# Optimization experiments

Hardware: AMD Instinct MI355X
Metric: run time of the kernel (lower is better)

The kernel has to match this reference:

```python
import jax, jax.numpy as jnp
import numpy as np

D_MODEL, D_STATE, D_CONV, D_INNER, DT_RANK = 1024, 16, 4, 2048, 64
B_SZ, L = 4, 2048

def setup_inputs() -> dict:
    key = jax.random.key(0)
    ks = jax.random.split(key, 7)
    return {
        "hidden_states": jax.random.normal(ks[0], (B_SZ, L, D_MODEL), jnp.float32),
        "in_proj_w": jax.random.normal(ks[1], (2 * D_INNER, D_MODEL), jnp.float32) * (D_MODEL ** -0.5),
        "conv_w": jax.random.normal(ks[2], (D_INNER, 1, D_CONV), jnp.float32) * 0.5,
        "conv_b": jax.random.normal(ks[3], (D_INNER,), jnp.float32) * 0.1,
        "x_proj_w": jax.random.normal(ks[4], (DT_RANK + 2 * D_STATE, D_INNER), jnp.float32) * (D_INNER ** -0.5),
        "dt_proj_w": jax.random.normal(ks[5], (D_INNER, DT_RANK), jnp.float32) * (DT_RANK ** -0.5),
        "A_log": jax.random.uniform(ks[6], (D_INNER, D_STATE), jnp.float32, 0.0, 2.0),
    }

def reference(hidden_states, in_proj_w, conv_w, conv_b, x_proj_w, dt_proj_w, A_log):
    b, l, d = hidden_states.shape
    # in_proj: (b,l,d) x (2*d_inner,d)^T -> (b, 2*d_inner, l)
    xz = jnp.einsum('bld,ed->bel', hidden_states, in_proj_w)
    x, z = jnp.split(xz, 2, axis=1)  # each (b, d_inner, l); z unused downstream
    A = -jnp.exp(A_log)              # (d_inner, d_state)
    # causal depthwise conv1d (left pad d_conv-1) + SiLU
    x = jax.lax.conv_general_dilated(
        x, conv_w, window_strides=(1,), padding=[(D_CONV - 1, 0)],
        feature_group_count=D_INNER,
        dimension_numbers=('NCH', 'OIH', 'NCH'))
    x = jax.nn.silu(x + conv_b[None, :, None])  # (b, d_inner, l)
    # x_proj: (b,l,dt_rank+2*d_state)
    x_dbl = jnp.einsum('bdl,ed->ble', x, x_proj_w)
    dt, B_mat, C_mat = jnp.split(x_dbl, [DT_RANK, DT_RANK + D_STATE], axis=-1)
    dt = jnp.einsum('blr,dr->bdl', dt, dt_proj_w)          # (b, d_inner, l), no bias
    B_mat = jnp.swapaxes(B_mat, 1, 2)                      # (b, d_state, l)
    C_mat = jnp.swapaxes(C_mat, 1, 2)                      # (b, d_state, l)
    return (dt, A, B_mat, C_mat, x)
```

## Files before the change

### kernel.cpp

```cpp
#include <hip/hip_runtime.h>
#include <hip/hip_bf16.h>
#include <math.h>

#define D_MODEL 1024
#define D_STATE 16
#define D_CONV  4
#define D_INNER 2048
#define DT_RANK 64
#define B_SZ    4
#define L_SEQ   2048

#define OFF_DT 0
#define OFF_A  (B_SZ * D_INNER * L_SEQ)
#define OFF_B  (OFF_A + D_INNER * D_STATE)
#define OFF_C  (OFF_B + B_SZ * D_STATE * L_SEQ)
#define OFF_X  (OFF_C + B_SZ * D_STATE * L_SEQ)

typedef __attribute__((ext_vector_type(8))) short bf16x8;
typedef __attribute__((ext_vector_type(8))) unsigned short us8;
typedef __attribute__((ext_vector_type(4))) float f32x4;
typedef unsigned short ushort_t;
typedef unsigned int uint_t;

static __device__ __forceinline__ ushort_t f2bf(float f) {
  __hip_bfloat16 h = __float2bfloat16(f);
  return *(ushort_t*)&h;
}
static __device__ __forceinline__ float bf2f(ushort_t u) {
  union { uint_t u; float f; } c;
  c.u = ((uint_t)u) << 16;
  return c.f;
}

#define N4_HS   (B_SZ * L_SEQ * D_MODEL / 4)
#define N4_W    (D_INNER * D_MODEL / 4)
#define N4_XW   ((DT_RANK + 2 * D_STATE) * D_INNER / 4)
#define N4_DW   (D_INNER * DT_RANK / 4)
#define N4_Z0   (B_SZ * DT_RANK * L_SEQ / 4)
#define N4_Z1   (2 * B_SZ * D_STATE * L_SEQ / 4)
#define N4_A    (D_INNER * D_STATE / 4)
#define N4_TOT  (N4_HS + N4_W + N4_XW + N4_DW + N4_Z0 + N4_Z1 + N4_A)

__global__ __launch_bounds__(256) void k_prep(
    const float4* __restrict__ hs, const float4* __restrict__ ipw,
    const float4* __restrict__ xpw, const float4* __restrict__ dpw,
    const float4* __restrict__ alog,
    ushort4* __restrict__ bfHS, ushort4* __restrict__ bfW,
    ushort4* __restrict__ xwb, ushort4* __restrict__ dwb,
    float4* __restrict__ z0, float4* __restrict__ z1,
    float4* __restrict__ aout) {
  int i = blockIdx.x * 256 + threadIdx.x;
  if (i < N4_HS) {
    float4 v = hs[i];
    ushort4 o; o.x = f2bf(v.x); o.y = f2bf(v.y); o.z = f2bf(v.z); o.w = f2bf(v.w);
    bfHS[i] = o;
    return;
  }
  i -= N4_HS;
  if (i < N4_W) {
    float4 v = ipw[i];
    ushort4 o; o.x = f2bf(v.x); o.y = f2bf(v.y); o.z = f2bf(v.z); o.w = f2bf(v.w);
    bfW[i] = o;
    return;
  }
  i -= N4_W;
  if (i < N4_XW) {
    float4 v = xpw[i];
    ushort4 o; o.x = f2bf(v.x); o.y = f2bf(v.y); o.z = f2bf(v.z); o.w = f2bf(v.w);
    xwb[i] = o;
    return;
  }
  i -= N4_XW;
  if (i < N4_DW) {
    float4 v = dpw[i];
    ushort4 o; o.x = f2bf(v.x); o.y = f2bf(v.y); o.z = f2bf(v.z); o.w = f2bf(v.w);
    dwb[i] = o;
    return;
  }
  i -= N4_DW;
  if (i < N4_Z0) { z0[i] = (float4){0.f, 0.f, 0.f, 0.f}; return; }
  i -= N4_Z0;
  if (i < N4_Z1) { z1[i] = (float4){0.f, 0.f, 0.f, 0.f}; return; }
  i -= N4_Z1;
  if (i < N4_A) {
    float4 v = alog[i];
    float4 o;
    o.x = -expf(v.x); o.y = -expf(v.y); o.z = -expf(v.z); o.w = -expf(v.w);
    aout[i] = o;
  }
}

__global__ __launch_bounds__(512, 2) void k_inproj_mfma(
    const ushort_t* __restrict__ Wb,
    const ushort_t* __restrict__ HSb,
    ushort_t* __restrict__ Cout) {
  const int flat = blockIdx.x + 8 * blockIdx.y + 64 * blockIdx.z;
  const int swz  = (flat & 7) * 32 + (flat >> 3);
  const int bn = swz & 7;
  const int bm = (swz >> 3) & 7;
  const int b  = swz >> 6;

  __shared__ ushort_t sh[65536];
  const int tid  = threadIdx.x;
  const int w    = tid >> 6;
  const int lane = tid & 63;
  const int wm = w >> 2, wn = w & 3;
  const int ksel = lane >> 4;
  const int frow = lane & 15;
  const int sr = tid >> 2;
  const int ss = tid & 3;

  const ushort_t* Ag = Wb + (size_t)(bm * 256) * D_MODEL;
  const ushort_t* Bg = HSb + (size_t)b * L_SEQ * D_MODEL
                           + (size_t)(bn * 256) * D_MODEL;

  f32x4 acc[8][4];
#pragma unroll
  for (int m = 0; m < 8; ++m)
#pragma unroll
    for (int n = 0; n < 4; ++n) acc[m][n] = (f32x4){0.f, 0.f, 0.f, 0.f};

  const int sxs = ss ^ ((sr >> 1) & 3);

#define STAGE(BUF, T)                                                            \
  do {                                                                           \
    _Pragma("unroll")                                                            \
    for (int mh = 0; mh < 4; ++mh) {                                             \
      const ushort_t* gbase = (mh < 2) ? Ag : Bg;                                \
      const ushort_t* grow = gbase + (size_t)((mh & 1) * 128 + sr) * D_MODEL     \
                                   + (T) * 64 + sxs * 8;                         \
      _Pragma("unroll")                                                          \
      for (int q = 0; q < 2; ++q) {                                              \
        ushort_t* dst = sh + (BUF) * 32768 + (mh >> 1) * 16384                   \
                           + (mh & 1) * 8192 + q * 4096 + tid * 8;               \
        __builtin_amdgcn_global_load_lds(                                        \
            (const __attribute__((address_space(1))) void*)(grow + q * 32),      \
            (__attribute__((address_space(3))) void*)dst, 16, 0, 0);             \
      }                                                                          \
    }                                                                            \
  } while (0)

#define COMPUTE(BUF)                                                             \
  do {                                                                           \
    _Pragma("unroll")                                                            \
    for (int ks = 0; ks < 2; ++ks) {                                             \
      bf16x8 af[8], bfr[4];                                                      \
      _Pragma("unroll")                                                          \
      for (int m = 0; m < 8; ++m) {                                              \
        int r = m * 16 + frow;                                                   \
        af[m] = *(const bf16x8*)(sh + (BUF) * 32768 + wm * 8192 + ks * 4096      \
                                 + (r * 4 + (ksel ^ ((r >> 1) & 3))) * 8);       \
      }                                                                          \
      _Pragma("unroll")                                                          \
      for (int n = 0; n < 4; ++n) {                                              \
        int ll = wn * 64 + n * 16 + frow;                                        \
        int h = ll >> 7, r = ll & 127;                                           \
        bfr[n] = *(const bf16x8*)(sh + (BUF) * 32768 + 16384 + h * 8192          \
                                  + ks * 4096                                    \
                                  + (r * 4 + (ksel ^ ((r >> 1) & 3))) * 8);      \
      }                                                                          \
      __builtin_amdgcn_s_setprio(1);                                             \
      _Pragma("unroll")                                                          \
      for (int m = 0; m < 8; ++m)                                                \
        _Pragma("unroll")                                                        \
        for (int n = 0; n < 4; ++n)                                              \
          acc[m][n] = __builtin_amdgcn_mfma_f32_16x16x32_bf16(af[m], bfr[n],     \
                                                              acc[m][n], 0, 0, 0); \
      __builtin_amdgcn_s_setprio(0);                                             \
    }                                                                            \
  } while (0)

  STAGE(0, 0);
  STAGE(1, 1);
  asm volatile("s_waitcnt vmcnt(8)" ::: "memory");
  __builtin_amdgcn_s_barrier();

  for (int t = 0; t < 14; ++t) {
    COMPUTE(t & 1);
    __builtin_amdgcn_sched_barrier(0);
    __builtin_amdgcn_s_barrier();
    STAGE(t & 1, t + 2);
    asm volatile("s_waitcnt vmcnt(8)" ::: "memory");
    __builtin_amdgcn_s_barrier();
    __builtin_amdgcn_sched_barrier(0);
  }
  COMPUTE(0);
  __builtin_amdgcn_sched_barrier(0);
  __builtin_amdgcn_s_barrier();
  asm volatile("s_waitcnt vmcnt(0)" ::: "memory");
  __builtin_amdgcn_s_barrier();
  COMPUTE(1);
#undef STAGE
#undef COMPUTE

  __syncthreads();

  const int crow0 = (lane >> 4) * 4;
  const int ccol  = lane & 15;
  ushort_t* Cb = Cout + (size_t)b * D_INNER * L_SEQ;
#pragma unroll
  for (int p = 0; p < 2; ++p) {
    if (wm == p) {
#pragma unroll
      for (int m = 0; m < 8; ++m)
#pragma unroll
        for (int n = 0; n < 4; ++n) {
          int r0 = m * 16 + crow0;
          int c  = wn * 64 + n * 16 + ccol;
#pragma unroll
          for (int i = 0; i < 4; ++i)
            sh[(r0 + i) * 272 + c] = f2bf(acc[m][n][i]);
        }
    }
    __syncthreads();
#pragma unroll
    for (int q = 0; q < 8; ++q) {
      int idx = q * 512 + tid;
      int r   = idx >> 5;
      int c8  = idx & 31;
      us8 v = *(const us8*)(sh + r * 272 + c8 * 8);
      *(us8*)(Cb + (size_t)(bm * 256 + p * 128 + r) * L_SEQ + bn * 256 + c8 * 8) = v;
    }
    __syncthreads();
  }
}

__global__ __launch_bounds__(256) void k_xproj_fused(
    const ushort_t* __restrict__ XWb,
    const ushort_t* __restrict__ Xpre,
    const float* __restrict__ CW,
    const float* __restrict__ CB,
    float* __restrict__ Xout,
    float* __restrict__ XDBL,
    float* __restrict__ OutB,
    float* __restrict__ OutC) {
  const int ln = blockIdx.x;
  const int sk = blockIdx.y;
  const int b  = blockIdx.z;
  __shared__ ushort_t As[96 * 40];
  __shared__ ushort_t Bs[64 * 34];
  const int tid  = threadIdx.x;
  const int wv   = tid >> 6;
  const int lane = tid & 63;
  const int wr = wv >> 1, wc = wv & 1;
  const int ksel = lane >> 4;
  const int frow = lane & 15;

  f32x4 acc[3][2];
#pragma unroll
  for (int i = 0; i < 3; ++i)
#pragma unroll
    for (int j = 0; j < 2; ++j) acc[i][j] = (f32x4){0.f, 0.f, 0.f, 0.f};

  for (int k0 = 0; k0 < 512; k0 += 32) {
    const int koff = sk * 512 + k0;
    {
      int row = tid >> 2, s = tid & 3;
      bf16x8 v = *(const bf16x8*)(XWb + (size_t)row * D_INNER + koff + s * 8);
      *(bf16x8*)(As + row * 40 + s * 8) = v;
      if (tid < 128) {
        int row2 = 64 + (tid >> 2);
        bf16x8 v2 = *(const bf16x8*)(XWb + (size_t)row2 * D_INNER + koff + s * 8);
        *(bf16x8*)(As + row2 * 40 + s * 8) = v2;
      }
    }
    {
      int n4 = tid & 15;
      int kp = tid >> 4;
      int l0 = ln * 64 + 4 * n4;
      float sv[2][4];
#pragma unroll
      for (int r = 0; r < 2; ++r) {
        int d = koff + 2 * kp + r;
        const ushort_t* row = Xpre + ((size_t)b * D_INNER + d) * L_SEQ;
        ushort4 cur = *(const ushort4*)(row + l0);
        float em3 = 0.f, em2 = 0.f, em1 = 0.f;
        if (l0 >= 4) {
          ushort4 pv = *(const ushort4*)(row + l0 - 4);
          em3 = bf2f(pv.y); em2 = bf2f(pv.z); em1 = bf2f(pv.w);
        }
        float ee[7] = {em3, em2, em1, bf2f(cur.x), bf2f(cur.y), bf2f(cur.z), bf2f(cur.w)};
        float4 w = *(const float4*)(CW + d * 4);
        float bias = CB[d];
#pragma unroll
        for (int i = 0; i < 4; ++i) {
          float v = w.x * ee[i] + w.y * ee[i + 1] + w.z * ee[i + 2] + w.w * ee[i + 3] + bias;
          sv[r][i] = v / (1.f + expf(-v));
        }
        *(float4*)(Xout + ((size_t)b * D_INNER + d) * L_SEQ + l0) =
            make_float4(sv[r][0], sv[r][1], sv[r][2], sv[r][3]);
      }
#pragma unroll
      for (int i = 0; i < 4; ++i) {
        uint_t pk = (uint_t)f2bf(sv[0][i]) | ((uint_t)f2bf(sv[1][i]) << 16);
        *(uint_t*)(Bs + (4 * n4 + i) * 34 + 2 * kp) = pk;
      }
    }
    __syncthreads();

    bf16x8 af[3], bfr[2];
#pragma unroll
    for (int mi = 0; mi < 3; ++mi) {
      int row = wr * 48 + mi * 16 + frow;
      af[mi] = *(const bf16x8*)(As + row * 40 + ksel * 8);
    }
#pragma unroll
    for (int ni = 0; ni < 2; ++ni) {
      int n = wc * 32 + ni * 16 + frow;
      const uint_t* p = (const uint_t*)(Bs + n * 34);
      union { uint_t u[4]; bf16x8 v; } fr;
#pragma unroll
      for (int q = 0; q < 4; ++q) fr.u[q] = p[ksel * 4 + q];
      bfr[ni] = fr.v;
    }
#pragma unroll
    for (int mi = 0; mi < 3; ++mi)
#pragma unroll
      for (int ni = 0; ni < 2; ++ni)
        acc[mi][ni] = __builtin_amdgcn_mfma_f32_16x16x32_bf16(af[mi], bfr[ni], acc[mi][ni], 0, 0, 0);
    __syncthreads();
  }

  const int crow0 = (lane >> 4) * 4;
  const int ccol  = lane & 15;
#pragma unroll
  for (int mi = 0; mi < 3; ++mi) {
    int e0 = wr * 48 + mi * 16 + crow0;
    float* base;
    int eoff;
    if (e0 < 64)      { base = XDBL + (size_t)b * 64 * L_SEQ; eoff = e0; }
    else if (e0 < 80) { base = OutB + (size_t)b * D_STATE * L_SEQ; eoff = e0 - 64; }
    else              { base = OutC + (size_t)b * D_STATE * L_SEQ; eoff = e0 - 80; }
#pragma unroll
    for (int ni = 0; ni < 2; ++ni) {
      int l = ln * 64 + wc * 32 + ni * 16 + ccol;
#pragma unroll
      for (int r = 0; r < 4; ++r)
        atomicAdd(base + (size_t)(eoff + r) * L_SEQ + l, acc[mi][ni][r]);
    }
  }
}

__global__ __launch_bounds__(256) void k_dt_mfma(
    const ushort_t* __restrict__ DWb,
    const float* __restrict__ XDBL,
    float* __restrict__ DT) {
  const int ln = blockIdx.x;
  const int dm = blockIdx.y;
  const int b  = blockIdx.z;
  __shared__ ushort_t As[128 * 72];
  __shared__ ushort_t Bs[128 * 68];
  const int tid  = threadIdx.x;
  const int wv   = tid >> 6;
  const int lane = tid & 63;
  const int wr = wv >> 1, wc = wv & 1;
  const int ksel = lane >> 4;
  const int frow = lane & 15;

#pragma unroll
  for (int q = 0; q < 4; ++q) {
    int u = tid + 256 * q;
    int row = u >> 3, s = u & 7;
    *(bf16x8*)(As + row * 72 + s * 8) =
        *(const bf16x8*)(DWb + (size_t)(dm * 128 + row) * DT_RANK + s * 8);
  }
#pragma unroll
  for (int q = 0; q < 4; ++q) {
    int u = tid + 256 * q;
    int n4 = u & 31;
    int kp = u >> 5;
    const float* g = XDBL + ((size_t)b * DT_RANK + 2 * kp) * L_SEQ + ln * 128 + 4 * n4;
    float4 x0 = *(const float4*)g;
    float4 x1 = *(const float4*)(g + L_SEQ);
    float e0[4] = {x0.x, x0.y, x0.z, x0.w};
    float e1[4] = {x1.x, x1.y, x1.z, x1.w};
#pragma unroll
    for (int i = 0; i < 4; ++i) {
      uint_t pk = (uint_t)f2bf(e0[i]) | ((uint_t)f2bf(e1[i]) << 16);
      *(uint_t*)(Bs + (4 * n4 + i) * 68 + 2 * kp) = pk;
    }
  }
  __syncthreads();

  f32x4 acc[4][4];
#pragma unroll
  for (int i = 0; i < 4; ++i)
#pragma unroll
    for (int j = 0; j < 4; ++j) acc[i][j] = (f32x4){0.f, 0.f, 0.f, 0.f};

#pragma unroll
  for (int ks = 0; ks < 2; ++ks) {
    bf16x8 af[4], bfr[4];
#pragma unroll
    for (int m = 0; m < 4; ++m) {
      int row = wr * 64 + m * 16 + frow;
      af[m] = *(const bf16x8*)(As + row * 72 + ks * 32 + ksel * 8);
    }
#pragma unroll
    for (int n = 0; n < 4; ++n) {
      int nn = wc * 64 + n * 16 + frow;
      bfr[n] = *(const bf16x8*)(Bs + nn * 68 + ks * 32 + ksel * 8);
    }
#pragma unroll
    for (int m = 0; m < 4; ++m)
#pragma unroll
      for (int n = 0; n < 4; ++n)
        acc[m][n] = __builtin_amdgcn_mfma_f32_16x16x32_bf16(af[m], bfr[n], acc[m][n], 0, 0, 0);
  }

  const int crow0 = (lane >> 4) * 4;
  const int ccol  = lane & 15;
  float* Cb = DT + (size_t)b * D_INNER * L_SEQ;
#pragma unroll
  for (int m = 0; m < 4; ++m) {
    int gr0 = dm * 128 + wr * 64 + m * 16 + crow0;
#pragma unroll
    for (int n = 0; n < 4; ++n) {
      int gc = ln * 128 + wc * 64 + n * 16 + ccol;
#pragma unroll
      for (int i = 0; i < 4; ++i)
        Cb[(size_t)(gr0 + i) * L_SEQ + gc] = acc[m][n][i];
    }
  }
}

extern "C" void kernel_launch(void* const* d_in, const int* in_sizes, int n_in,
                              void* d_out, int out_size, void* d_ws, size_t ws_size,
                              hipStream_t stream) {
  const float* hs   = (const float*)d_in[0];
  const float* ipw  = (const float*)d_in[1];
  const float* cw   = (const float*)d_in[2];
  const float* cb   = (const float*)d_in[3];
  const float* xpw  = (const float*)d_in[4];
  const float* dpw  = (const float*)d_in[5];
  const float* alog = (const float*)d_in[6];

  float* out    = (float*)d_out;
  float* dt_out = out + OFF_DT;
  float* a_out  = out + OFF_A;
  float* b_out  = out + OFF_B;
  float* c_out  = out + OFF_C;
  float* x_out  = out + OFF_X;

  unsigned short* bfHS = (unsigned short*)x_out;
  unsigned short* bfW  = bfHS + (size_t)B_SZ * L_SEQ * D_MODEL;
  unsigned short* xpre = (unsigned short*)dt_out;
  float* xdbl = (float*)d_ws;
  unsigned short* xwb = (unsigned short*)((char*)d_ws + 2097152);
  unsigned short* dwb = (unsigned short*)((char*)d_ws + 2097152 + 393216);

  k_prep<<<dim3((N4_TOT + 255) / 256), 256, 0, stream>>>(
      (const float4*)hs, (const float4*)ipw, (const float4*)xpw,
      (const float4*)dpw, (const float4*)alog,
      (ushort4*)bfHS, (ushort4*)bfW, (ushort4*)xwb, (ushort4*)dwb,
      (float4*)xdbl, (float4*)b_out, (float4*)a_out);

  k_inproj_mfma<<<dim3(8, 8, 4), 512, 0, stream>>>(bfW, bfHS, xpre);
  k_xproj_fused<<<dim3(32, 4, 4), 256, 0, stream>>>(xwb, xpre, cw, cb,
                                                    x_out, xdbl, b_out, c_out);
  k_dt_mfma<<<dim3(16, 16, 4), 256, 0, stream>>>(dwb, xdbl, dt_out);
}
```

Measured before the change: 119.8 us.

## Replace split-K atomics in x_proj with partial buffers reduced in dt kernel

```diff
diff --git a/kernel.cpp b/kernel.cpp
--- a/kernel.cpp
+++ b/kernel.cpp
@@ -36,10 +36,8 @@
 #define N4_W    (D_INNER * D_MODEL / 4)
 #define N4_XW   ((DT_RANK + 2 * D_STATE) * D_INNER / 4)
 #define N4_DW   (D_INNER * DT_RANK / 4)
-#define N4_Z0   (B_SZ * DT_RANK * L_SEQ / 4)
-#define N4_Z1   (2 * B_SZ * D_STATE * L_SEQ / 4)
 #define N4_A    (D_INNER * D_STATE / 4)
-#define N4_TOT  (N4_HS + N4_W + N4_XW + N4_DW + N4_Z0 + N4_Z1 + N4_A)
+#define N4_TOT  (N4_HS + N4_W + N4_XW + N4_DW + N4_A)
 
 __global__ __launch_bounds__(256) void k_prep(
     const float4* __restrict__ hs, const float4* __restrict__ ipw,
@@ -47,7 +45,6 @@
     const float4* __restrict__ alog,
     ushort4* __restrict__ bfHS, ushort4* __restrict__ bfW,
     ushort4* __restrict__ xwb, ushort4* __restrict__ dwb,
-    float4* __restrict__ z0, float4* __restrict__ z1,
     float4* __restrict__ aout) {
   int i = blockIdx.x * 256 + threadIdx.x;
   if (i < N4_HS) {
@@ -78,10 +75,6 @@
     return;
   }
   i -= N4_DW;
-  if (i < N4_Z0) { z0[i] = (float4){0.f, 0.f, 0.f, 0.f}; return; }
-  i -= N4_Z0;
-  if (i < N4_Z1) { z1[i] = (float4){0.f, 0.f, 0.f, 0.f}; return; }
-  i -= N4_Z1;
   if (i < N4_A) {
     float4 v = alog[i];
     float4 o;
@@ -231,9 +224,8 @@
     const float* __restrict__ CW,
     const float* __restrict__ CB,
     float* __restrict__ Xout,
-    float* __restrict__ XDBL,
-    float* __restrict__ OutB,
-    float* __restrict__ OutC) {
+    float* __restrict__ PX,
+    float* __restrict__ PBC) {
   const int ln = blockIdx.x;
   const int sk = blockIdx.y;
   const int b  = blockIdx.z;
@@ -328,23 +320,25 @@
     int e0 = wr * 48 + mi * 16 + crow0;
     float* base;
     int eoff;
-    if (e0 < 64)      { base = XDBL + (size_t)b * 64 * L_SEQ; eoff = e0; }
-    else if (e0 < 80) { base = OutB + (size_t)b * D_STATE * L_SEQ; eoff = e0 - 64; }
-    else              { base = OutC + (size_t)b * D_STATE * L_SEQ; eoff = e0 - 80; }
+    if (e0 < 64) { base = PX  + ((size_t)(sk * B_SZ + b) * 64) * L_SEQ; eoff = e0; }
+    else         { base = PBC + ((size_t)(sk * B_SZ + b) * 32) * L_SEQ; eoff = e0 - 64; }
 #pragma unroll
     for (int ni = 0; ni < 2; ++ni) {
       int l = ln * 64 + wc * 32 + ni * 16 + ccol;
 #pragma unroll
       for (int r = 0; r < 4; ++r)
-        atomicAdd(base + (size_t)(eoff + r) * L_SEQ + l, acc[mi][ni][r]);
+        base[(size_t)(eoff + r) * L_SEQ + l] = acc[mi][ni][r];
     }
   }
 }
 
 __global__ __launch_bounds__(256) void k_dt_mfma(
     const ushort_t* __restrict__ DWb,
-    const float* __restrict__ XDBL,
-    float* __restrict__ DT) {
+    const float* __restrict__ PX,
+    const float* __restrict__ PBC,
+    float* __restrict__ DT,
+    float* __restrict__ OutB,
+    float* __restrict__ OutC) {
   const int ln = blockIdx.x;
   const int dm = blockIdx.y;
   const int b  = blockIdx.z;
@@ -369,9 +363,16 @@
     int u = tid + 256 * q;
     int n4 = u & 31;
     int kp = u >> 5;
-    const float* g = XDBL + ((size_t)b * DT_RANK + 2 * kp) * L_SEQ + ln * 128 + 4 * n4;
-    float4 x0 = *(const float4*)g;
-    float4 x1 = *(const float4*)(g + L_SEQ);
+    float4 x0 = {0.f, 0.f, 0.f, 0.f}, x1 = {0.f, 0.f, 0.f, 0.f};
+#pragma unroll
+    for (int sk = 0; sk < 4; ++sk) {
+      const float* g = PX + ((size_t)(sk * B_SZ + b) * 64 + 2 * kp) * L_SEQ
+                          + ln * 128 + 4 * n4;
+      float4 a0 = *(const float4*)g;
+      float4 a1 = *(const float4*)(g + L_SEQ);
+      x0.x += a0.x; x0.y += a0.y; x0.z += a0.z; x0.w += a0.w;
+      x1.x += a1.x; x1.y += a1.y; x1.z += a1.z; x1.w += a1.w;
+    }
     float e0[4] = {x0.x, x0.y, x0.z, x0.w};
     float e1[4] = {x1.x, x1.y, x1.z, x1.w};
 #pragma unroll
@@ -420,6 +421,26 @@
 #pragma unroll
       for (int i = 0; i < 4; ++i)
         Cb[(size_t)(gr0 + i) * L_SEQ + gc] = acc[m][n][i];
+    }
+  }
+
+  if (dm == 0) {
+#pragma unroll
+    for (int q = 0; q < 4; ++q) {
+      int u = tid + 256 * q;
+      int e  = u >> 5;
+      int c4 = u & 31;
+      int l0 = ln * 128 + c4 * 4;
+      float4 s = {0.f, 0.f, 0.f, 0.f};
+#pragma unroll
+      for (int sk = 0; sk < 4; ++sk) {
+        float4 p = *(const float4*)(PBC + ((size_t)(sk * B_SZ + b) * 32 + e) * L_SEQ + l0);
+        s.x += p.x; s.y += p.y; s.z += p.z; s.w += p.w;
+      }
+      if (e < 16)
+        *(float4*)(OutB + ((size_t)b * D_STATE + e) * L_SEQ + l0) = s;
+      else
+        *(float4*)(OutC + ((size_t)b * D_STATE + (e - 16)) * L_SEQ + l0) = s;
     }
   }
 }
@@ -445,18 +466,20 @@
   unsigned short* bfHS = (unsigned short*)x_out;
   unsigned short* bfW  = bfHS + (size_t)B_SZ * L_SEQ * D_MODEL;
   unsigned short* xpre = (unsigned short*)dt_out;
-  float* xdbl = (float*)d_ws;
-  unsigned short* xwb = (unsigned short*)((char*)d_ws + 2097152);
-  unsigned short* dwb = (unsigned short*)((char*)d_ws + 2097152 + 393216);
+  float* px  = (float*)d_ws;
+  float* pbc = (float*)((char*)d_ws + 8388608);
+  unsigned short* xwb = (unsigned short*)((char*)d_ws + 8388608 + 4194304);
+  unsigned short* dwb = (unsigned short*)((char*)d_ws + 8388608 + 4194304 + 393216);
 
   k_prep<<<dim3((N4_TOT + 255) / 256), 256, 0, stream>>>(
       (const float4*)hs, (const float4*)ipw, (const float4*)xpw,
       (const float4*)dpw, (const float4*)alog,
       (ushort4*)bfHS, (ushort4*)bfW, (ushort4*)xwb, (ushort4*)dwb,
-      (float4*)xdbl, (float4*)b_out, (float4*)a_out);
+      (float4*)a_out);
 
   k_inproj_mfma<<<dim3(8, 8, 4), 512, 0, stream>>>(bfW, bfHS, xpre);
   k_xproj_fused<<<dim3(32, 4, 4), 256, 0, stream>>>(xwb, xpre, cw, cb,
-                                                    x_out, xdbl, b_out, c_out);
-  k_dt_mfma<<<dim3(16, 16, 4), 256, 0, stream>>>(dwb, xdbl, dt_out);
-}
+                                                    x_out, px, pbc);
+  k_dt_mfma<<<dim3(16, 16, 4), 256, 0, stream>>>(dwb, px, pbc, dt_out,
+                                                 b_out, c_out);
+}
```

After: 122.5 us. +2.3%, slower.
